# Optimization experiments

Hardware: AMD Instinct MI355X
Metric: run time of the kernel (lower is better)

## Reference

```python
import jax, jax.numpy as jnp
import numpy as np
import math

D_MODEL = 512
N_HEAD = 8
HEAD_DIM = D_MODEL // N_HEAD


def _rel_sinusoid(seq_len, dim):
    # Sinusoidal embedding for relative positions -seq_len .. seq_len-1, shape [2L, dim]
    half = dim // 2
    inv_freq = jnp.exp(jnp.arange(half, dtype=jnp.float32) * (-math.log(10000.0) / (half - 1)))
    ang = jnp.arange(-seq_len, seq_len, dtype=jnp.float32)[:, None] * inv_freq[None, :]
    return jnp.concatenate([jnp.sin(ang), jnp.cos(ang)], axis=1)  # [2L, dim]


def _shift(BD):
    # Transformer-XL shift trick: [b, n, L, 2L] -> [b, n, L, L]
    b, n, L, _ = BD.shape
    BD = jnp.concatenate([BD, jnp.zeros((b, n, L, 1), BD.dtype)], axis=-1)  # [b,n,L,2L+1]
    BD = BD.reshape(b, n, -1, L)[:, :, :-1].reshape(b, n, L, -1)  # [b,n,L,2L]
    return BD[:, :, :, L:]


def setup_inputs() -> dict:
    key = jax.random.key(0)
    ks = jax.random.split(key, 6)
    B, L = 8, 1024
    x = jax.random.normal(ks[0], (B, L, D_MODEL), jnp.float32)
    mask = jax.random.randint(ks[1], (B, L), 0, 2).astype(jnp.int32)
    W_qkv = jax.random.normal(ks[2], (D_MODEL, 3 * D_MODEL), jnp.float32) / math.sqrt(D_MODEL)
    r_r_bias = jax.random.normal(ks[3], (N_HEAD, HEAD_DIM), jnp.float32) * 0.1
    r_w_bias = jax.random.normal(ks[4], (N_HEAD, HEAD_DIM), jnp.float32) * 0.1
    w_kr = jax.random.normal(ks[5], (HEAD_DIM, HEAD_DIM), jnp.float32) * 0.1
    return {"x": x, "mask": mask, "W_qkv": W_qkv, "r_r_bias": r_r_bias, "r_w_bias": r_w_bias, "w_kr": w_kr}


def reference(x, mask, W_qkv, r_r_bias, r_w_bias, w_kr):
    B, L, d_model = x.shape
    scale = math.sqrt(HEAD_DIM)
    pos_embed = _rel_sinusoid(L, HEAD_DIM)  # [2L, head_dim]

    qkv = x @ W_qkv  # [B, L, 3*d_model]
    q, k, v = jnp.split(qkv, 3, axis=-1)
    q = q.reshape(B, L, N_HEAD, HEAD_DIM).transpose(0, 2, 1, 3)  # [B, H, L, hd]
    k = k.reshape(B, L, N_HEAD, HEAD_DIM).transpose(0, 2, 1, 3)
    v = v.reshape(B, L, N_HEAD, HEAD_DIM).transpose(0, 2, 1, 3)

    rw_head_q = q + r_r_bias[None, :, None, :]
    AC = jnp.einsum('bnqd,bnkd->bnqk', rw_head_q, k)  # [B,H,L,L]

    rel = pos_embed @ w_kr  # [2L, hd]
    D_ = jnp.einsum('nd,ld->nl', r_w_bias, rel)[None, :, None, :]  # [1,H,1,2L]
    B_ = jnp.einsum('bnqd,ld->bnql', q, rel)  # [B,H,L,2L]
    BD = _shift(B_ + D_)  # [B,H,L,L]

    attn = (AC + BD) / scale
    attn = jnp.where(mask[:, None, None, :] == 0, jnp.float32(1e-9), attn)
    attn = jax.nn.softmax(attn, axis=-1)  # dropout is identity at eval

    out = jnp.einsum('bnqk,bnkd->bnqd', attn, v)  # [B,H,L,hd]
    return out.transpose(0, 2, 1, 3).reshape(B, L, d_model)
```

## Files before the change

kernel.cpp:

```cpp
#include <hip/hip_runtime.h>
#include <hip/hip_bf16.h>
#include <stdint.h>

typedef __bf16 bf16x8 __attribute__((ext_vector_type(8)));
typedef float  f32x4  __attribute__((ext_vector_type(4)));

#define D_MODEL 512
#define N_HEAD  8
#define HD      64
#define L_      1024
#define SCALE   0.125f
#define EXP_NEG8 3.35462628e-4f
#define L2E     1.44269504f
#define NEG8L2E -11.54156036f

__device__ __forceinline__ unsigned short f2bf(float f) {
  unsigned int u = __builtin_bit_cast(unsigned int, f);
  u += 0x7FFFu + ((u >> 16) & 1u);
  return (unsigned short)(u >> 16);
}
__device__ __forceinline__ float bf2f(unsigned short h) {
  unsigned int u = ((unsigned int)h) << 16;
  return __builtin_bit_cast(float, u);
}

__device__ __forceinline__ void gld_lds16(const void* g, void* l) {
  __builtin_amdgcn_global_load_lds(
      (const __attribute__((address_space(1))) void*)g,
      (__attribute__((address_space(3))) void*)l, 16, 0, 0);
}
__device__ __forceinline__ void gld_lds4(const void* g, void* l) {
  __builtin_amdgcn_global_load_lds(
      (const __attribute__((address_space(1))) void*)g,
      (__attribute__((address_space(3))) void*)l, 4, 0, 0);
}

__global__ __launch_bounds__(256) void k_cvt_x(const float* __restrict__ x,
                                               unsigned short* __restrict__ xbf) {
  int t = blockIdx.x * 256 + threadIdx.x;
  const float4* p = reinterpret_cast<const float4*>(x) + (size_t)t * 2;
  float4 a = p[0], b = p[1];
  ushort4 o0 = { f2bf(a.x), f2bf(a.y), f2bf(a.z), f2bf(a.w) };
  ushort4 o1 = { f2bf(b.x), f2bf(b.y), f2bf(b.z), f2bf(b.w) };
  ushort4* q = reinterpret_cast<ushort4*>(xbf) + (size_t)t * 2;
  q[0] = o0; q[1] = o1;
}

__global__ __launch_bounds__(256) void k_cvt_wt(const float* __restrict__ W,
                                                unsigned short* __restrict__ Wt) {
  __shared__ float tile[32][33];
  int kb = blockIdx.x;
  int nb = blockIdx.y;
  int t = threadIdx.x;
  int r = t >> 3, c4 = (t & 7) * 4;
  float4 v = *reinterpret_cast<const float4*>(W + (size_t)(kb * 32 + r) * 1536 + nb * 32 + c4);
  tile[r][c4 + 0] = v.x; tile[r][c4 + 1] = v.y; tile[r][c4 + 2] = v.z; tile[r][c4 + 3] = v.w;
  __syncthreads();
  int a = t >> 3, b4 = (t & 7) * 4;
  ushort4 o = { f2bf(tile[b4 + 0][a]), f2bf(tile[b4 + 1][a]),
                f2bf(tile[b4 + 2][a]), f2bf(tile[b4 + 3][a]) };
  *reinterpret_cast<ushort4*>(Wt + (size_t)(nb * 32 + a) * 512 + kb * 32 + b4) = o;
}

__global__ __launch_bounds__(256) void k_stab(float* __restrict__ SCF,
                                              unsigned short* __restrict__ SBF) {
  int tid = blockIdx.x * 256 + threadIdx.x;
  int l = tid >> 6, d = tid & 63;
  const float kInv = -9.210340371976184f / 31.0f;
  float f = expf((float)(d & 31) * kInv);
  float ang = (float)l * f;
  float v = (d < 32) ? sinf(ang) : cosf(ang);
  SCF[tid] = v;
  SBF[tid] = f2bf(v);
}

__global__ __launch_bounds__(256) void k_wz(const unsigned short* __restrict__ Wt,
                                            const float* __restrict__ wkr,
                                            const float* __restrict__ rwb,
                                            unsigned short* __restrict__ Wzt,
                                            float* __restrict__ CZ) {
  __shared__ float wkrS[64][64];
  __shared__ float panS[64][36];
  int blk = blockIdx.x;
  int h = blk >> 4, kc = blk & 15;
  int t = threadIdx.x;
  for (int i = t; i < 4096; i += 256) wkrS[i >> 6][i & 63] = wkr[i];
  {
    int d = t >> 2, j0 = (t & 3) * 8;
    const unsigned short* src = Wt + (size_t)(h * 64 + d) * 512 + kc * 32 + j0;
    for (int j = 0; j < 8; ++j) panS[d][j0 + j] = bf2f(src[j]);
  }
  __syncthreads();
  int e = t >> 2, j0 = (t & 3) * 8;
  float acc[8];
  for (int j = 0; j < 8; ++j) acc[j] = 0.f;
  for (int d = 0; d < 64; ++d) {
    float wv = wkrS[e][d];
    for (int j = 0; j < 8; ++j) acc[j] += wv * panS[d][j0 + j];
  }
  unsigned short* dst = Wzt + (size_t)(h * 64 + e) * 512 + kc * 32 + j0;
  ushort4 o0 = { f2bf(acc[0]), f2bf(acc[1]), f2bf(acc[2]), f2bf(acc[3]) };
  ushort4 o1 = { f2bf(acc[4]), f2bf(acc[5]), f2bf(acc[6]), f2bf(acc[7]) };
  *reinterpret_cast<ushort4*>(dst) = o0;
  *reinterpret_cast<ushort4*>(dst + 4) = o1;
  if (kc == 0 && t < 64) {
    float c = 0.f;
    for (int d = 0; d < 64; ++d) c += wkrS[t][d] * rwb[h * 64 + d];
    CZ[h * 64 + t] = c;
  }
}

__global__ __launch_bounds__(256, 3) void k_gemm_qkv(const unsigned short* __restrict__ Xbf,
                                                     const unsigned short* __restrict__ Wt,
                                                     const float* __restrict__ rrb,
                                                     const float* __restrict__ SCF,
                                                     const float* __restrict__ CZ,
                                                     unsigned short* __restrict__ QKV,
                                                     unsigned short* __restrict__ Vt,
                                                     unsigned short* __restrict__ Aq) {
  __shared__ unsigned short As[2][128][32];
  __shared__ unsigned short Bs[2][128][32];
  int lin = blockIdx.y * 64 + blockIdx.x;
  int xcd = lin & 7, idx = lin >> 3;
  int bx = xcd * 8 + idx / 16;
  int by = idx % 16;
  int m0 = bx * 128;
  int n0 = by * 128;
  int w = threadIdx.x >> 6, lane = threadIdx.x & 63;
  int lr = lane & 15, g = lane >> 4;
  int wm = (w >> 1) * 64, wn = (w & 1) * 64;
  int srow = lane >> 2, schk = (lane & 3) * 8;

  auto stage = [&](int buf, int k0) {
#pragma unroll
    for (int j = 0; j < 2; ++j) {
      int row = w * 32 + j * 16 + srow;
      gld_lds16(Xbf + (size_t)(m0 + row) * 512 + k0 + schk, &As[buf][w * 32 + j * 16][0]);
      gld_lds16(Wt  + (size_t)(n0 + row) * 512 + k0 + schk, &Bs[buf][w * 32 + j * 16][0]);
    }
  };

  f32x4 acc[4][4];
  for (int i = 0; i < 4; ++i) for (int j = 0; j < 4; ++j) acc[i][j] = (f32x4){0.f, 0.f, 0.f, 0.f};

  stage(0, 0);
  __syncthreads();

  for (int it = 0; it < 16; ++it) {
    int cur = it & 1;
    if (it < 15) stage(cur ^ 1, (it + 1) * 32);
    bf16x8 a[4], b[4];
#pragma unroll
    for (int mt = 0; mt < 4; ++mt)
      a[mt] = __builtin_bit_cast(bf16x8, *reinterpret_cast<const uint4*>(&As[cur][wm + mt * 16 + lr][g * 8]));
#pragma unroll
    for (int nt = 0; nt < 4; ++nt)
      b[nt] = __builtin_bit_cast(bf16x8, *reinterpret_cast<const uint4*>(&Bs[cur][wn + nt * 16 + lr][g * 8]));
#pragma unroll
    for (int mt = 0; mt < 4; ++mt)
#pragma unroll
      for (int nt = 0; nt < 4; ++nt)
        acc[mt][nt] = __builtin_amdgcn_mfma_f32_16x16x32_bf16(a[mt], b[nt], acc[mt][nt], 0, 0, 0);
    __syncthreads();
  }

  int region = n0 >> 9;
  if (region == 3) {
    int nvb = (n0 - 1536) + wn;
    int h = nvb >> 6;
    int bb = m0 >> 10;
    float cz0 = CZ[nvb + lr];
    float cz1 = CZ[nvb + 16 + lr];
    float cz2 = CZ[nvb + 32 + lr];
    float cz3 = CZ[nvb + 48 + lr];
#pragma unroll
    for (int mt = 0; mt < 4; ++mt)
#pragma unroll
      for (int r = 0; r < 4; ++r) {
        int m = m0 + wm + mt * 16 + g * 4 + r;
        int lrow = m & 1023;
        const float* sc = SCF + (size_t)lrow * 64;
        float s0 = sc[lr], s1 = sc[16 + lr], c0 = sc[32 + lr], c1 = sc[48 + lr];
        float z0 = acc[mt][0][r] + cz0;
        float z1 = acc[mt][1][r] + cz1;
        float z2 = acc[mt][2][r] + cz2;
        float z3 = acc[mt][3][r] + cz3;
        unsigned short* ap = Aq + ((size_t)(bb * 8 + h) * 1024 + lrow) * 64;
        ap[lr]      = f2bf((z0 * c0 + z2 * s0) * SCALE);
        ap[16 + lr] = f2bf((z1 * c1 + z3 * s1) * SCALE);
        ap[32 + lr] = f2bf((z2 * c0 - z0 * s0) * SCALE);
        ap[48 + lr] = f2bf((z3 * c1 - z1 * s1) * SCALE);
      }
  } else if (region == 2) {
#pragma unroll
    for (int mt = 0; mt < 4; ++mt)
#pragma unroll
      for (int nt = 0; nt < 4; ++nt) {
        int m = m0 + wm + mt * 16 + g * 4;
        int n = n0 + wn + nt * 16 + lr;
        int nv = n - 1024;
        int bb = m >> 10, h = nv >> 6, d = nv & 63;
        ushort4 o = { f2bf(acc[mt][nt][0]), f2bf(acc[mt][nt][1]),
                      f2bf(acc[mt][nt][2]), f2bf(acc[mt][nt][3]) };
        *reinterpret_cast<ushort4*>(Vt + (size_t)((bb * 8 + h) * 64 + d) * 1024 + (m & 1023)) = o;
      }
  } else if (region == 0) {
#pragma unroll
    for (int mt = 0; mt < 4; ++mt)
#pragma unroll
      for (int nt = 0; nt < 4; ++nt) {
        int n = n0 + wn + nt * 16 + lr;
        float bias = rrb[n];
#pragma unroll
        for (int r = 0; r < 4; ++r) {
          int m = m0 + wm + mt * 16 + g * 4 + r;
          QKV[(size_t)m * 1536 + n] = f2bf((acc[mt][nt][r] + bias) * SCALE);
        }
      }
  } else {
#pragma unroll
    for (int mt = 0; mt < 4; ++mt)
#pragma unroll
      for (int nt = 0; nt < 4; ++nt)
#pragma unroll
        for (int r = 0; r < 4; ++r) {
          int m = m0 + wm + mt * 16 + g * 4 + r;
          int n = n0 + wn + nt * 16 + lr;
          QKV[(size_t)m * 1536 + n] = f2bf(acc[mt][nt][r]);
        }
  }
}

__global__ __launch_bounds__(256, 3) void k_attn(const unsigned short* __restrict__ QKV,
                                                 const unsigned short* __restrict__ Vt,
                                                 const unsigned short* __restrict__ Sbf,
                                                 const unsigned short* __restrict__ Aq,
                                                 const int* __restrict__ mask,
                                                 float* __restrict__ out) {
  __shared__ unsigned short KtS[2][64][64];
  __shared__ unsigned short VtS[2][64][64];
  __shared__ int MtS[2][64];
  __shared__ unsigned short pS[4][32][64];

  int n_ = blockIdx.x;
  int l = (n_ & 7) * 64 + (n_ >> 3);
  int bh = l >> 3, qt = l & 7;
  int b = bh >> 3, h = bh & 7;
  int w = threadIdx.x >> 6, lane = threadIdx.x & 63;
  int lr = lane & 15, g = lane >> 4;
  int qw0 = qt * 128 + w * 32;
  int rsub = lane >> 3;
  int csub = (lane & 7) ^ rsub;
  int swz = lr & 7;

  bf16x8 qrr[2][2], qa[2][2];
#pragma unroll
  for (int mt = 0; mt < 2; ++mt) {
    const unsigned short* qrow = QKV + (size_t)(b * L_ + qw0 + mt * 16 + lr) * 1536 + h * HD;
    const unsigned short* arow = Aq + ((size_t)bh * L_ + qw0 + mt * 16 + lr) * HD;
#pragma unroll
    for (int ks = 0; ks < 2; ++ks) {
      qrr[mt][ks] = __builtin_bit_cast(bf16x8, *reinterpret_cast<const uint4*>(qrow + ks * 32 + g * 8));
      qa[mt][ks]  = __builtin_bit_cast(bf16x8, *reinterpret_cast<const uint4*>(arow + ks * 32 + g * 8));
    }
  }

  auto stage = [&](int nb, int k0n) {
#pragma unroll
    for (int j = 0; j < 2; ++j) {
      int row = w * 16 + j * 8;
      const unsigned short* gK = QKV + (size_t)(b * L_ + k0n + row + rsub) * 1536 +
                                 D_MODEL + h * HD + csub * 8;
      gld_lds16(gK, &KtS[nb][row][0]);
      const unsigned short* gV = Vt + (size_t)(bh * HD + row + rsub) * L_ + k0n + csub * 8;
      gld_lds16(gV, &VtS[nb][row][0]);
    }
    if (w == 0) gld_lds4(mask + b * L_ + k0n + lane, &MtS[nb][0]);
  };

  stage(0, 0);

  float lsum[2] = {0.f, 0.f};
  f32x4 accO[2][4];
#pragma unroll
  for (int mt = 0; mt < 2; ++mt)
#pragma unroll
    for (int nt = 0; nt < 4; ++nt) accO[mt][nt] = (f32x4){0.f, 0.f, 0.f, 0.f};

  char* psw = (char*)&pS[w][0][0];
  __syncthreads();

  for (int it = 0; it < 16; ++it) {
    int k0 = it << 6;
    int cur = it & 1;
    if (it < 15) stage(cur ^ 1, k0 + 64);

    bf16x8 sf[4][2];
#pragma unroll
    for (int t4 = 0; t4 < 4; ++t4)
#pragma unroll
      for (int ks = 0; ks < 2; ++ks)
        sf[t4][ks] = __builtin_bit_cast(bf16x8, *reinterpret_cast<const uint4*>(
            Sbf + (size_t)(k0 + t4 * 16 + lr) * HD + ks * 32 + g * 8));

    f32x4 ac[2][4];
#pragma unroll
    for (int mt = 0; mt < 2; ++mt)
#pragma unroll
      for (int t4 = 0; t4 < 4; ++t4) ac[mt][t4] = (f32x4){0.f, 0.f, 0.f, 0.f};
#pragma unroll
    for (int t4 = 0; t4 < 4; ++t4) {
#pragma unroll
      for (int ks = 0; ks < 2; ++ks) {
        const unsigned short* kp = &KtS[cur][t4 * 16 + lr][((((ks << 2) | g) ^ swz) << 3)];
        bf16x8 kfr = __builtin_bit_cast(bf16x8, *reinterpret_cast<const uint4*>(kp));
        ac[0][t4] = __builtin_amdgcn_mfma_f32_16x16x32_bf16(kfr, qrr[0][ks], ac[0][t4], 0, 0, 0);
        ac[1][t4] = __builtin_amdgcn_mfma_f32_16x16x32_bf16(kfr, qrr[1][ks], ac[1][t4], 0, 0, 0);
      }
#pragma unroll
      for (int ks = 0; ks < 2; ++ks) {
        ac[0][t4] = __builtin_amdgcn_mfma_f32_16x16x32_bf16(sf[t4][ks], qa[0][ks], ac[0][t4], 0, 0, 0);
        ac[1][t4] = __builtin_amdgcn_mfma_f32_16x16x32_bf16(sf[t4][ks], qa[1][ks], ac[1][t4], 0, 0, 0);
      }
    }

#pragma unroll
    for (int t4 = 0; t4 < 4; ++t4) {
      int4 mk = *reinterpret_cast<const int4*>(&MtS[cur][t4 * 16 + g * 4]);
#pragma unroll
      for (int mt = 0; mt < 2; ++mt) {
        float e0 = __builtin_amdgcn_exp2f(fmaf(ac[mt][t4][0], L2E, NEG8L2E));
        float e1 = __builtin_amdgcn_exp2f(fmaf(ac[mt][t4][1], L2E, NEG8L2E));
        float e2 = __builtin_amdgcn_exp2f(fmaf(ac[mt][t4][2], L2E, NEG8L2E));
        float e3 = __builtin_amdgcn_exp2f(fmaf(ac[mt][t4][3], L2E, NEG8L2E));
        e0 = mk.x ? e0 : EXP_NEG8;
        e1 = mk.y ? e1 : EXP_NEG8;
        e2 = mk.z ? e2 : EXP_NEG8;
        e3 = mk.w ? e3 : EXP_NEG8;
        lsum[mt] += (e0 + e1) + (e2 + e3);
        unsigned int lo, hi;
        asm("v_cvt_pk_bf16_f32 %0, %1, %2" : "=v"(lo) : "v"(e0), "v"(e1));
        asm("v_cvt_pk_bf16_f32 %0, %1, %2" : "=v"(hi) : "v"(e2), "v"(e3));
        uint2 pk; pk.x = lo; pk.y = hi;
        *reinterpret_cast<uint2*>(psw + ((mt * 16 + lr) * 128 +
            (((t4 << 5) | (g << 3)) ^ (swz << 4)))) = pk;
      }
    }

    bf16x8 pa[2][2];
#pragma unroll
    for (int mt = 0; mt < 2; ++mt)
#pragma unroll
      for (int ks = 0; ks < 2; ++ks)
        pa[mt][ks] = __builtin_bit_cast(bf16x8, *reinterpret_cast<const uint4*>(
            psw + ((mt * 16 + lr) * 128 + (((ks << 6) | (g << 4)) ^ (swz << 4)))));
#pragma unroll
    for (int nt = 0; nt < 4; ++nt)
#pragma unroll
      for (int ks = 0; ks < 2; ++ks) {
        const unsigned short* vp = &VtS[cur][nt * 16 + lr][((((ks << 2) | g) ^ swz) << 3)];
        bf16x8 vfr = __builtin_bit_cast(bf16x8, *reinterpret_cast<const uint4*>(vp));
        accO[0][nt] = __builtin_amdgcn_mfma_f32_16x16x32_bf16(pa[0][ks], vfr, accO[0][nt], 0, 0, 0);
        accO[1][nt] = __builtin_amdgcn_mfma_f32_16x16x32_bf16(pa[1][ks], vfr, accO[1][nt], 0, 0, 0);
      }
    __syncthreads();
  }

#pragma unroll
  for (int mt = 0; mt < 2; ++mt) {
    lsum[mt] += __shfl_xor(lsum[mt], 16);
    lsum[mt] += __shfl_xor(lsum[mt], 32);
  }
  float dsum[2][4];
#pragma unroll
  for (int mt = 0; mt < 2; ++mt)
#pragma unroll
    for (int r = 0; r < 4; ++r) dsum[mt][r] = __shfl(lsum[mt], g * 4 + r);

#pragma unroll
  for (int mt = 0; mt < 2; ++mt)
#pragma unroll
    for (int nt = 0; nt < 4; ++nt)
#pragma unroll
      for (int r = 0; r < 4; ++r) {
        int q = qw0 + mt * 16 + g * 4 + r;
        out[(size_t)(b * L_ + q) * D_MODEL + h * HD + nt * 16 + lr] = accO[mt][nt][r] / dsum[mt][r];
      }
}

extern "C" void kernel_launch(void* const* d_in, const int* in_sizes, int n_in,
                              void* d_out, int out_size, void* d_ws, size_t ws_size,
                              hipStream_t stream) {
  const float* x    = (const float*)d_in[0];
  const int*   mask = (const int*)d_in[1];
  const float* Wqkv = (const float*)d_in[2];
  const float* rrb  = (const float*)d_in[3];
  const float* rwb  = (const float*)d_in[4];
  const float* wkr  = (const float*)d_in[5];
  float* out = (float*)d_out;

  char* ws = (char*)d_ws;
  size_t off = 0;
  unsigned short* XBF = (unsigned short*)(ws + off); off += (size_t)8192 * 512 * 2;
  unsigned short* WT  = (unsigned short*)(ws + off); off += (size_t)2048 * 512 * 2;
  unsigned short* QKV = (unsigned short*)(ws + off); off += (size_t)8192 * 1536 * 2;
  unsigned short* VT  = (unsigned short*)(ws + off); off += (size_t)64 * 64 * 1024 * 2;
  unsigned short* AQ  = (unsigned short*)(ws + off); off += (size_t)64 * 1024 * 64 * 2;
  float*          SCF = (float*)(ws + off);          off += (size_t)1024 * 64 * 4;
  unsigned short* SBF = (unsigned short*)(ws + off); off += (size_t)1024 * 64 * 2;
  float*          CZ  = (float*)(ws + off);          off += 512 * 4;

  hipLaunchKernelGGL(k_cvt_x,    dim3(2048),   dim3(256), 0, stream, x, XBF);
  hipLaunchKernelGGL(k_cvt_wt,   dim3(16, 48), dim3(256), 0, stream, Wqkv, WT);
  hipLaunchKernelGGL(k_stab,     dim3(256),    dim3(256), 0, stream, SCF, SBF);
  hipLaunchKernelGGL(k_wz,       dim3(128),    dim3(256), 0, stream, WT, wkr, rwb, WT + (size_t)1536 * 512, CZ);
  hipLaunchKernelGGL(k_gemm_qkv, dim3(64, 16), dim3(256), 0, stream, XBF, WT, rrb, SCF, CZ, QKV, VT, AQ);
  hipLaunchKernelGGL(k_attn,     dim3(512),    dim3(256), 0, stream, QKV, VT, SBF, AQ, mask, out);
}
```

Measured before the change: 92.75 us.

## Widen QKV GEMM tile to 128x256 and double attention block query rows

The QKV projection GEMM now computes 128x256 output tiles, with each wave covering 64x128, which halves the grid and doubles B-operand reuse per A load. The epilogues are adapted, including the rotary-style z transform, which now loops over two heads per wave. The attention kernel moves to 512-thread blocks covering 256 query rows each, so every staged K/V tile is shared by eight waves instead of four. The cost is higher register pressure and fewer blocks (512 GEMM blocks, 256 attention blocks), which may leave CUs underfilled on a 256-CU part.

```diff
diff --git a/kernel.cpp b/kernel.cpp
--- a/kernel.cpp
+++ b/kernel.cpp
@@ -110,7 +110,7 @@
   }
 }
 
-__global__ __launch_bounds__(256, 3) void k_gemm_qkv(const unsigned short* __restrict__ Xbf,
+__global__ __launch_bounds__(256, 2) void k_gemm_qkv(const unsigned short* __restrict__ Xbf,
                                                      const unsigned short* __restrict__ Wt,
                                                      const float* __restrict__ rrb,
                                                      const float* __restrict__ SCF,
@@ -119,29 +119,33 @@
                                                      unsigned short* __restrict__ Vt,
                                                      unsigned short* __restrict__ Aq) {
   __shared__ unsigned short As[2][128][32];
-  __shared__ unsigned short Bs[2][128][32];
+  __shared__ unsigned short Bs[2][256][32];
   int lin = blockIdx.y * 64 + blockIdx.x;
   int xcd = lin & 7, idx = lin >> 3;
-  int bx = xcd * 8 + idx / 16;
-  int by = idx % 16;
+  int bx = xcd * 8 + (idx >> 3);
+  int by = idx & 7;
   int m0 = bx * 128;
-  int n0 = by * 128;
+  int n0 = by * 256;
   int w = threadIdx.x >> 6, lane = threadIdx.x & 63;
   int lr = lane & 15, g = lane >> 4;
-  int wm = (w >> 1) * 64, wn = (w & 1) * 64;
+  int wm = (w >> 1) * 64, wn = (w & 1) * 128;
   int srow = lane >> 2, schk = (lane & 3) * 8;
 
   auto stage = [&](int buf, int k0) {
 #pragma unroll
     for (int j = 0; j < 2; ++j) {
-      int row = w * 32 + j * 16 + srow;
-      gld_lds16(Xbf + (size_t)(m0 + row) * 512 + k0 + schk, &As[buf][w * 32 + j * 16][0]);
-      gld_lds16(Wt  + (size_t)(n0 + row) * 512 + k0 + schk, &Bs[buf][w * 32 + j * 16][0]);
+      int row = w * 32 + j * 16;
+      gld_lds16(Xbf + (size_t)(m0 + row + srow) * 512 + k0 + schk, &As[buf][row][0]);
+    }
+#pragma unroll
+    for (int j = 0; j < 4; ++j) {
+      int row = w * 64 + j * 16;
+      gld_lds16(Wt + (size_t)(n0 + row + srow) * 512 + k0 + schk, &Bs[buf][row][0]);
     }
   };
 
-  f32x4 acc[4][4];
-  for (int i = 0; i < 4; ++i) for (int j = 0; j < 4; ++j) acc[i][j] = (f32x4){0.f, 0.f, 0.f, 0.f};
+  f32x4 acc[4][8];
+  for (int i = 0; i < 4; ++i) for (int j = 0; j < 8; ++j) acc[i][j] = (f32x4){0.f, 0.f, 0.f, 0.f};
 
   stage(0, 0);
   __syncthreads();
@@ -149,53 +153,57 @@
   for (int it = 0; it < 16; ++it) {
     int cur = it & 1;
     if (it < 15) stage(cur ^ 1, (it + 1) * 32);
-    bf16x8 a[4], b[4];
+    bf16x8 a[4], b[8];
 #pragma unroll
     for (int mt = 0; mt < 4; ++mt)
       a[mt] = __builtin_bit_cast(bf16x8, *reinterpret_cast<const uint4*>(&As[cur][wm + mt * 16 + lr][g * 8]));
 #pragma unroll
-    for (int nt = 0; nt < 4; ++nt)
+    for (int nt = 0; nt < 8; ++nt)
       b[nt] = __builtin_bit_cast(bf16x8, *reinterpret_cast<const uint4*>(&Bs[cur][wn + nt * 16 + lr][g * 8]));
 #pragma unroll
     for (int mt = 0; mt < 4; ++mt)
 #pragma unroll
-      for (int nt = 0; nt < 4; ++nt)
+      for (int nt = 0; nt < 8; ++nt)
         acc[mt][nt] = __builtin_amdgcn_mfma_f32_16x16x32_bf16(a[mt], b[nt], acc[mt][nt], 0, 0, 0);
     __syncthreads();
   }
 
   int region = n0 >> 9;
   if (region == 3) {
-    int nvb = (n0 - 1536) + wn;
-    int h = nvb >> 6;
+    int zb = (n0 - 1536) + wn;
     int bb = m0 >> 10;
-    float cz0 = CZ[nvb + lr];
-    float cz1 = CZ[nvb + 16 + lr];
-    float cz2 = CZ[nvb + 32 + lr];
-    float cz3 = CZ[nvb + 48 + lr];
+#pragma unroll
+    for (int hg = 0; hg < 2; ++hg) {
+      int hb = zb + hg * 64;
+      int h = hb >> 6;
+      float cz0 = CZ[hb + lr];
+      float cz1 = CZ[hb + 16 + lr];
+      float cz2 = CZ[hb + 32 + lr];
+      float cz3 = CZ[hb + 48 + lr];
+#pragma unroll
+      for (int mt = 0; mt < 4; ++mt)
+#pragma unroll
+        for (int r = 0; r < 4; ++r) {
+          int m = m0 + wm + mt * 16 + g * 4 + r;
+          int lrow = m & 1023;
+          const float* sc = SCF + (size_t)lrow * 64;
+          float s0 = sc[lr], s1 = sc[16 + lr], c0 = sc[32 + lr], c1 = sc[48 + lr];
+          float z0 = acc[mt][hg * 4 + 0][r] + cz0;
+          float z1 = acc[mt][hg * 4 + 1][r] + cz1;
+          float z2 = acc[mt][hg * 4 + 2][r] + cz2;
+          float z3 = acc[mt][hg * 4 + 3][r] + cz3;
+          unsigned short* ap = Aq + ((size_t)(bb * 8 + h) * 1024 + lrow) * 64;
+          ap[lr]      = f2bf((z0 * c0 + z2 * s0) * SCALE);
+          ap[16 + lr] = f2bf((z1 * c1 + z3 * s1) * SCALE);
+          ap[32 + lr] = f2bf((z2 * c0 - z0 * s0) * SCALE);
+          ap[48 + lr] = f2bf((z3 * c1 - z1 * s1) * SCALE);
+        }
+    }
+  } else if (region == 2) {
 #pragma unroll
     for (int mt = 0; mt < 4; ++mt)
 #pragma unroll
-      for (int r = 0; r < 4; ++r) {
-        int m = m0 + wm + mt * 16 + g * 4 + r;
-        int lrow = m & 1023;
-        const float* sc = SCF + (size_t)lrow * 64;
-        float s0 = sc[lr], s1 = sc[16 + lr], c0 = sc[32 + lr], c1 = sc[48 + lr];
-        float z0 = acc[mt][0][r] + cz0;
-        float z1 = acc[mt][1][r] + cz1;
-        float z2 = acc[mt][2][r] + cz2;
-        float z3 = acc[mt][3][r] + cz3;
-        unsigned short* ap = Aq + ((size_t)(bb * 8 + h) * 1024 + lrow) * 64;
-        ap[lr]      = f2bf((z0 * c0 + z2 * s0) * SCALE);
-        ap[16 + lr] = f2bf((z1 * c1 + z3 * s1) * SCALE);
-        ap[32 + lr] = f2bf((z2 * c0 - z0 * s0) * SCALE);
-        ap[48 + lr] = f2bf((z3 * c1 - z1 * s1) * SCALE);
-      }
-  } else if (region == 2) {
-#pragma unroll
-    for (int mt = 0; mt < 4; ++mt)
-#pragma unroll
-      for (int nt = 0; nt < 4; ++nt) {
+      for (int nt = 0; nt < 8; ++nt) {
         int m = m0 + wm + mt * 16 + g * 4;
         int n = n0 + wn + nt * 16 + lr;
         int nv = n - 1024;
@@ -208,7 +216,7 @@
 #pragma unroll
     for (int mt = 0; mt < 4; ++mt)
 #pragma unroll
-      for (int nt = 0; nt < 4; ++nt) {
+      for (int nt = 0; nt < 8; ++nt) {
         int n = n0 + wn + nt * 16 + lr;
         float bias = rrb[n];
 #pragma unroll
@@ -221,7 +229,7 @@
 #pragma unroll
     for (int mt = 0; mt < 4; ++mt)
 #pragma unroll
-      for (int nt = 0; nt < 4; ++nt)
+      for (int nt = 0; nt < 8; ++nt)
 #pragma unroll
         for (int r = 0; r < 4; ++r) {
           int m = m0 + wm + mt * 16 + g * 4 + r;
@@ -231,7 +239,7 @@
   }
 }
 
-__global__ __launch_bounds__(256, 3) void k_attn(const unsigned short* __restrict__ QKV,
+__global__ __launch_bounds__(512, 2) void k_attn(const unsigned short* __restrict__ QKV,
                                                  const unsigned short* __restrict__ Vt,
                                                  const unsigned short* __restrict__ Sbf,
                                                  const unsigned short* __restrict__ Aq,
@@ -240,15 +248,15 @@
   __shared__ unsigned short KtS[2][64][64];
   __shared__ unsigned short VtS[2][64][64];
   __shared__ int MtS[2][64];
-  __shared__ unsigned short pS[4][32][64];
+  __shared__ unsigned short pS[8][32][64];
 
   int n_ = blockIdx.x;
-  int l = (n_ & 7) * 64 + (n_ >> 3);
-  int bh = l >> 3, qt = l & 7;
+  int l = (n_ & 7) * 32 + (n_ >> 3);
+  int bh = l >> 2, qt = l & 3;
   int b = bh >> 3, h = bh & 7;
   int w = threadIdx.x >> 6, lane = threadIdx.x & 63;
   int lr = lane & 15, g = lane >> 4;
-  int qw0 = qt * 128 + w * 32;
+  int qw0 = qt * 256 + w * 32;
   int rsub = lane >> 3;
   int csub = (lane & 7) ^ rsub;
   int swz = lr & 7;
@@ -266,15 +274,12 @@
   }
 
   auto stage = [&](int nb, int k0n) {
-#pragma unroll
-    for (int j = 0; j < 2; ++j) {
-      int row = w * 16 + j * 8;
-      const unsigned short* gK = QKV + (size_t)(b * L_ + k0n + row + rsub) * 1536 +
-                                 D_MODEL + h * HD + csub * 8;
-      gld_lds16(gK, &KtS[nb][row][0]);
-      const unsigned short* gV = Vt + (size_t)(bh * HD + row + rsub) * L_ + k0n + csub * 8;
-      gld_lds16(gV, &VtS[nb][row][0]);
-    }
+    int row = w * 8;
+    const unsigned short* gK = QKV + (size_t)(b * L_ + k0n + row + rsub) * 1536 +
+                               D_MODEL + h * HD + csub * 8;
+    gld_lds16(gK, &KtS[nb][row][0]);
+    const unsigned short* gV = Vt + (size_t)(bh * HD + row + rsub) * L_ + k0n + csub * 8;
+    gld_lds16(gV, &VtS[nb][row][0]);
     if (w == 0) gld_lds4(mask + b * L_ + k0n + lane, &MtS[nb][0]);
   };
 
@@ -414,6 +419,6 @@
   hipLaunchKernelGGL(k_cvt_wt,   dim3(16, 48), dim3(256), 0, stream, Wqkv, WT);
   hipLaunchKernelGGL(k_stab,     dim3(256),    dim3(256), 0, stream, SCF, SBF);
   hipLaunchKernelGGL(k_wz,       dim3(128),    dim3(256), 0, stream, WT, wkr, rwb, WT + (size_t)1536 * 512, CZ);
-  hipLaunchKernelGGL(k_gemm_qkv, dim3(64, 16), dim3(256), 0, stream, XBF, WT, rrb, SCF, CZ, QKV, VT, AQ);
-  hipLaunchKernelGGL(k_attn,     dim3(512),    dim3(256), 0, stream, QKV, VT, SBF, AQ, mask, out);
-}
+  hipLaunchKernelGGL(k_gemm_qkv, dim3(64, 8),  dim3(256), 0, stream, XBF, WT, rrb, SCF, CZ, QKV, VT, AQ);
+  hipLaunchKernelGGL(k_attn,     dim3(256),    dim3(512), 0, stream, QKV, VT, SBF, AQ, mask, out);
+}
```

Measured after the change: 107.3 us. 15.7% more time.

## Split attention over key halves with atomic accumulation and separate normalization

Applied to the files above, without the earlier changes.

Splits each attention block's key range into two halves, which doubles the grid to 1024 blocks and raises the occupancy hint to 4 blocks per SM. Partial outputs are accumulated into the zeroed output with float atomics, and partial row sums go to a workspace that a new normalization kernel reads to divide the output. V fragments are now loaded directly from global memory instead of being staged through shared memory, which reduces LDS usage. The cost is a memset, atomic traffic, an extra kernel launch and a second pass over the output.

```diff
diff --git a/kernel.cpp b/kernel.cpp
--- a/kernel.cpp
+++ b/kernel.cpp
@@ -231,21 +231,24 @@
   }
 }
 
-__global__ __launch_bounds__(256, 3) void k_attn(const unsigned short* __restrict__ QKV,
+__global__ __launch_bounds__(256, 4) void k_attn(const unsigned short* __restrict__ QKV,
                                                  const unsigned short* __restrict__ Vt,
                                                  const unsigned short* __restrict__ Sbf,
                                                  const unsigned short* __restrict__ Aq,
                                                  const int* __restrict__ mask,
-                                                 float* __restrict__ out) {
+                                                 float* __restrict__ out,
+                                                 float* __restrict__ Lp) {
   __shared__ unsigned short KtS[2][64][64];
-  __shared__ unsigned short VtS[2][64][64];
   __shared__ int MtS[2][64];
   __shared__ unsigned short pS[4][32][64];
 
   int n_ = blockIdx.x;
-  int l = (n_ & 7) * 64 + (n_ >> 3);
-  int bh = l >> 3, qt = l & 7;
+  int xcd = n_ & 7, idx = n_ >> 3;
+  int bh = xcd * 8 + (idx >> 4);
+  int rem = idx & 15;
+  int qt = rem >> 1, kh = rem & 1;
   int b = bh >> 3, h = bh & 7;
+  int kbase = kh << 9;
   int w = threadIdx.x >> 6, lane = threadIdx.x & 63;
   int lr = lane & 15, g = lane >> 4;
   int qw0 = qt * 128 + w * 32;
@@ -272,13 +275,11 @@
       const unsigned short* gK = QKV + (size_t)(b * L_ + k0n + row + rsub) * 1536 +
                                  D_MODEL + h * HD + csub * 8;
       gld_lds16(gK, &KtS[nb][row][0]);
-      const unsigned short* gV = Vt + (size_t)(bh * HD + row + rsub) * L_ + k0n + csub * 8;
-      gld_lds16(gV, &VtS[nb][row][0]);
     }
     if (w == 0) gld_lds4(mask + b * L_ + k0n + lane, &MtS[nb][0]);
   };
 
-  stage(0, 0);
+  stage(0, kbase);
 
   float lsum[2] = {0.f, 0.f};
   f32x4 accO[2][4];
@@ -290,10 +291,10 @@
   char* psw = (char*)&pS[w][0][0];
   __syncthreads();
 
-  for (int it = 0; it < 16; ++it) {
-    int k0 = it << 6;
+  for (int it = 0; it < 8; ++it) {
+    int k0 = kbase + (it << 6);
     int cur = it & 1;
-    if (it < 15) stage(cur ^ 1, k0 + 64);
+    if (it < 7) stage(cur ^ 1, k0 + 64);
 
     bf16x8 sf[4][2];
 #pragma unroll
@@ -302,6 +303,14 @@
       for (int ks = 0; ks < 2; ++ks)
         sf[t4][ks] = __builtin_bit_cast(bf16x8, *reinterpret_cast<const uint4*>(
             Sbf + (size_t)(k0 + t4 * 16 + lr) * HD + ks * 32 + g * 8));
+
+    bf16x8 vfr[4][2];
+#pragma unroll
+    for (int nt = 0; nt < 4; ++nt)
+#pragma unroll
+      for (int ks = 0; ks < 2; ++ks)
+        vfr[nt][ks] = __builtin_bit_cast(bf16x8, *reinterpret_cast<const uint4*>(
+            Vt + (size_t)(bh * HD + nt * 16 + lr) * L_ + k0 + ks * 32 + g * 8));
 
     f32x4 ac[2][4];
 #pragma unroll
@@ -358,10 +367,8 @@
     for (int nt = 0; nt < 4; ++nt)
 #pragma unroll
       for (int ks = 0; ks < 2; ++ks) {
-        const unsigned short* vp = &VtS[cur][nt * 16 + lr][((((ks << 2) | g) ^ swz) << 3)];
-        bf16x8 vfr = __builtin_bit_cast(bf16x8, *reinterpret_cast<const uint4*>(vp));
-        accO[0][nt] = __builtin_amdgcn_mfma_f32_16x16x32_bf16(pa[0][ks], vfr, accO[0][nt], 0, 0, 0);
-        accO[1][nt] = __builtin_amdgcn_mfma_f32_16x16x32_bf16(pa[1][ks], vfr, accO[1][nt], 0, 0, 0);
+        accO[0][nt] = __builtin_amdgcn_mfma_f32_16x16x32_bf16(pa[0][ks], vfr[nt][ks], accO[0][nt], 0, 0, 0);
+        accO[1][nt] = __builtin_amdgcn_mfma_f32_16x16x32_bf16(pa[1][ks], vfr[nt][ks], accO[1][nt], 0, 0, 0);
       }
     __syncthreads();
   }
@@ -371,11 +378,11 @@
     lsum[mt] += __shfl_xor(lsum[mt], 16);
     lsum[mt] += __shfl_xor(lsum[mt], 32);
   }
-  float dsum[2][4];
-#pragma unroll
-  for (int mt = 0; mt < 2; ++mt)
-#pragma unroll
-    for (int r = 0; r < 4; ++r) dsum[mt][r] = __shfl(lsum[mt], g * 4 + r);
+  if (g == 0) {
+#pragma unroll
+    for (int mt = 0; mt < 2; ++mt)
+      Lp[(size_t)kh * 65536 + bh * 1024 + qw0 + mt * 16 + lr] = lsum[mt];
+  }
 
 #pragma unroll
   for (int mt = 0; mt < 2; ++mt)
@@ -384,8 +391,23 @@
 #pragma unroll
       for (int r = 0; r < 4; ++r) {
         int q = qw0 + mt * 16 + g * 4 + r;
-        out[(size_t)(b * L_ + q) * D_MODEL + h * HD + nt * 16 + lr] = accO[mt][nt][r] / dsum[mt][r];
-      }
+        atomicAdd(&out[(size_t)(b * L_ + q) * D_MODEL + h * HD + nt * 16 + lr], accO[mt][nt][r]);
+      }
+}
+
+__global__ __launch_bounds__(256) void k_norm(float* __restrict__ out,
+                                              const float* __restrict__ Lp) {
+  int t = blockIdx.x * 256 + threadIdx.x;
+  int row = t >> 6;
+  int h = (t & 63) >> 3;
+  int b = row >> 10, q = row & 1023;
+  float l = Lp[(size_t)(b * 8 + h) * 1024 + q] + Lp[65536 + (size_t)(b * 8 + h) * 1024 + q];
+  float inv = 1.0f / l;
+  float4* p = reinterpret_cast<float4*>(out) + (size_t)t * 2;
+  float4 v0 = p[0], v1 = p[1];
+  v0.x *= inv; v0.y *= inv; v0.z *= inv; v0.w *= inv;
+  v1.x *= inv; v1.y *= inv; v1.z *= inv; v1.w *= inv;
+  p[0] = v0; p[1] = v1;
 }
 
 extern "C" void kernel_launch(void* const* d_in, const int* in_sizes, int n_in,
@@ -409,11 +431,14 @@
   float*          SCF = (float*)(ws + off);          off += (size_t)1024 * 64 * 4;
   unsigned short* SBF = (unsigned short*)(ws + off); off += (size_t)1024 * 64 * 2;
   float*          CZ  = (float*)(ws + off);          off += 512 * 4;
-
+  float*          LP  = (float*)(ws + off);          off += (size_t)2 * 65536 * 4;
+
+  hipMemsetAsync(out, 0, (size_t)out_size * sizeof(float), stream);
   hipLaunchKernelGGL(k_cvt_x,    dim3(2048),   dim3(256), 0, stream, x, XBF);
   hipLaunchKernelGGL(k_cvt_wt,   dim3(16, 48), dim3(256), 0, stream, Wqkv, WT);
   hipLaunchKernelGGL(k_stab,     dim3(256),    dim3(256), 0, stream, SCF, SBF);
   hipLaunchKernelGGL(k_wz,       dim3(128),    dim3(256), 0, stream, WT, wkr, rwb, WT + (size_t)1536 * 512, CZ);
   hipLaunchKernelGGL(k_gemm_qkv, dim3(64, 16), dim3(256), 0, stream, XBF, WT, rrb, SCF, CZ, QKV, VT, AQ);
-  hipLaunchKernelGGL(k_attn,     dim3(512),    dim3(256), 0, stream, QKV, VT, SBF, AQ, mask, out);
-}
+  hipLaunchKernelGGL(k_attn,     dim3(1024),   dim3(256), 0, stream, QKV, VT, SBF, AQ, mask, out, LP);
+  hipLaunchKernelGGL(k_norm,     dim3(2048),   dim3(256), 0, stream, out, LP);
+}
```

After: 186.6 us. 2.01x slower.

## Prefetch S fragments a tile ahead, read mask from global, add MFMA priority

Applied to the files above, without the earlier changes.

The attention loop now double-buffers the relative-position S fragments in registers, loading the next tile's fragments during the current iteration, with the loop unrolled by two to alternate buffers. The mask is read directly from global into registers instead of staged through LDS. s_setprio brackets the MFMA sections. Occupancy hint drops from 3 to 2 blocks per CU, giving more registers for the extra prefetch buffers at the cost of fewer resident waves.

```diff
diff --git a/kernel.cpp b/kernel.cpp
--- a/kernel.cpp
+++ b/kernel.cpp
@@ -28,11 +28,6 @@
   __builtin_amdgcn_global_load_lds(
       (const __attribute__((address_space(1))) void*)g,
       (__attribute__((address_space(3))) void*)l, 16, 0, 0);
-}
-__device__ __forceinline__ void gld_lds4(const void* g, void* l) {
-  __builtin_amdgcn_global_load_lds(
-      (const __attribute__((address_space(1))) void*)g,
-      (__attribute__((address_space(3))) void*)l, 4, 0, 0);
 }
 
 __global__ __launch_bounds__(256) void k_cvt_x(const float* __restrict__ x,
@@ -231,7 +226,7 @@
   }
 }
 
-__global__ __launch_bounds__(256, 3) void k_attn(const unsigned short* __restrict__ QKV,
+__global__ __launch_bounds__(256, 2) void k_attn(const unsigned short* __restrict__ QKV,
                                                  const unsigned short* __restrict__ Vt,
                                                  const unsigned short* __restrict__ Sbf,
                                                  const unsigned short* __restrict__ Aq,
@@ -239,7 +234,6 @@
                                                  float* __restrict__ out) {
   __shared__ unsigned short KtS[2][64][64];
   __shared__ unsigned short VtS[2][64][64];
-  __shared__ int MtS[2][64];
   __shared__ unsigned short pS[4][32][64];
 
   int n_ = blockIdx.x;
@@ -275,10 +269,15 @@
       const unsigned short* gV = Vt + (size_t)(bh * HD + row + rsub) * L_ + k0n + csub * 8;
       gld_lds16(gV, &VtS[nb][row][0]);
     }
-    if (w == 0) gld_lds4(mask + b * L_ + k0n + lane, &MtS[nb][0]);
   };
-
-  stage(0, 0);
+  auto loadSF = [&](int k0n, bf16x8 (&sf)[4][2]) {
+#pragma unroll
+    for (int t4 = 0; t4 < 4; ++t4)
+#pragma unroll
+      for (int ks = 0; ks < 2; ++ks)
+        sf[t4][ks] = __builtin_bit_cast(bf16x8, *reinterpret_cast<const uint4*>(
+            Sbf + (size_t)(k0n + t4 * 16 + lr) * HD + ks * 32 + g * 8));
+  };
 
   float lsum[2] = {0.f, 0.f};
   f32x4 accO[2][4];
@@ -288,26 +287,28 @@
     for (int nt = 0; nt < 4; ++nt) accO[mt][nt] = (f32x4){0.f, 0.f, 0.f, 0.f};
 
   char* psw = (char*)&pS[w][0][0];
+
+  bf16x8 sfA[4][2], sfB[4][2];
+  stage(0, 0);
+  loadSF(0, sfA);
   __syncthreads();
 
-  for (int it = 0; it < 16; ++it) {
+  auto iter = [&](int it, bf16x8 (&sfC)[4][2], bf16x8 (&sfN)[4][2]) {
     int k0 = it << 6;
     int cur = it & 1;
-    if (it < 15) stage(cur ^ 1, k0 + 64);
-
-    bf16x8 sf[4][2];
+    if (it < 15) { stage(cur ^ 1, k0 + 64); loadSF(k0 + 64, sfN); }
+
+    int4 mk[4];
 #pragma unroll
     for (int t4 = 0; t4 < 4; ++t4)
-#pragma unroll
-      for (int ks = 0; ks < 2; ++ks)
-        sf[t4][ks] = __builtin_bit_cast(bf16x8, *reinterpret_cast<const uint4*>(
-            Sbf + (size_t)(k0 + t4 * 16 + lr) * HD + ks * 32 + g * 8));
+      mk[t4] = *reinterpret_cast<const int4*>(mask + b * L_ + k0 + t4 * 16 + g * 4);
 
     f32x4 ac[2][4];
 #pragma unroll
     for (int mt = 0; mt < 2; ++mt)
 #pragma unroll
       for (int t4 = 0; t4 < 4; ++t4) ac[mt][t4] = (f32x4){0.f, 0.f, 0.f, 0.f};
+    __builtin_amdgcn_s_setprio(1);
 #pragma unroll
     for (int t4 = 0; t4 < 4; ++t4) {
 #pragma unroll
@@ -319,24 +320,24 @@
       }
 #pragma unroll
       for (int ks = 0; ks < 2; ++ks) {
-        ac[0][t4] = __builtin_amdgcn_mfma_f32_16x16x32_bf16(sf[t4][ks], qa[0][ks], ac[0][t4], 0, 0, 0);
-        ac[1][t4] = __builtin_amdgcn_mfma_f32_16x16x32_bf16(sf[t4][ks], qa[1][ks], ac[1][t4], 0, 0, 0);
+        ac[0][t4] = __builtin_amdgcn_mfma_f32_16x16x32_bf16(sfC[t4][ks], qa[0][ks], ac[0][t4], 0, 0, 0);
+        ac[1][t4] = __builtin_amdgcn_mfma_f32_16x16x32_bf16(sfC[t4][ks], qa[1][ks], ac[1][t4], 0, 0, 0);
       }
     }
+    __builtin_amdgcn_s_setprio(0);
 
 #pragma unroll
     for (int t4 = 0; t4 < 4; ++t4) {
-      int4 mk = *reinterpret_cast<const int4*>(&MtS[cur][t4 * 16 + g * 4]);
 #pragma unroll
       for (int mt = 0; mt < 2; ++mt) {
         float e0 = __builtin_amdgcn_exp2f(fmaf(ac[mt][t4][0], L2E, NEG8L2E));
         float e1 = __builtin_amdgcn_exp2f(fmaf(ac[mt][t4][1], L2E, NEG8L2E));
         float e2 = __builtin_amdgcn_exp2f(fmaf(ac[mt][t4][2], L2E, NEG8L2E));
         float e3 = __builtin_amdgcn_exp2f(fmaf(ac[mt][t4][3], L2E, NEG8L2E));
-        e0 = mk.x ? e0 : EXP_NEG8;
-        e1 = mk.y ? e1 : EXP_NEG8;
-        e2 = mk.z ? e2 : EXP_NEG8;
-        e3 = mk.w ? e3 : EXP_NEG8;
+        e0 = mk[t4].x ? e0 : EXP_NEG8;
+        e1 = mk[t4].y ? e1 : EXP_NEG8;
+        e2 = mk[t4].z ? e2 : EXP_NEG8;
+        e3 = mk[t4].w ? e3 : EXP_NEG8;
         lsum[mt] += (e0 + e1) + (e2 + e3);
         unsigned int lo, hi;
         asm("v_cvt_pk_bf16_f32 %0, %1, %2" : "=v"(lo) : "v"(e0), "v"(e1));
@@ -354,6 +355,7 @@
       for (int ks = 0; ks < 2; ++ks)
         pa[mt][ks] = __builtin_bit_cast(bf16x8, *reinterpret_cast<const uint4*>(
             psw + ((mt * 16 + lr) * 128 + (((ks << 6) | (g << 4)) ^ (swz << 4)))));
+    __builtin_amdgcn_s_setprio(1);
 #pragma unroll
     for (int nt = 0; nt < 4; ++nt)
 #pragma unroll
@@ -363,7 +365,13 @@
         accO[0][nt] = __builtin_amdgcn_mfma_f32_16x16x32_bf16(pa[0][ks], vfr, accO[0][nt], 0, 0, 0);
         accO[1][nt] = __builtin_amdgcn_mfma_f32_16x16x32_bf16(pa[1][ks], vfr, accO[1][nt], 0, 0, 0);
       }
+    __builtin_amdgcn_s_setprio(0);
     __syncthreads();
+  };
+
+  for (int base = 0; base < 16; base += 2) {
+    iter(base, sfA, sfB);
+    iter(base + 1, sfB, sfA);
   }
 
 #pragma unroll
```

New measurement: 95.86 us. +3.4%, slower.
